# Kernel tuning notes

Hardware: AMD Instinct MI355X
Metric: run time of the kernel (lower is better)

Reference implementation:

```python
import jax, jax.numpy as jnp
import numpy as np

G, K = 60, 13  # SO(3) group size, neighbors per group element


def _gather(x, nei):
    # x: [N, C, G] -> [N, C, G, K] via fixed neighbor indices (len G*K)
    return x[:, :, nei].reshape(x.shape[0], x.shape[1], G, K)


def _comb(x, nei, W, b):
    # gather-then-(1,K)-Conv2d == contraction over (channel, neighbor)
    d = _gather(x, nei)                                   # [N,C,G,K]
    return jnp.einsum('ncgk,ock->nog', d, W) + b[None, :, None]


def setup_inputs() -> dict:
    key = jax.random.key(0)
    ks = jax.random.split(key, 8)
    N = 512
    feats = jax.random.normal(ks[0], (N, 32, G), jnp.float32)
    nei = jax.random.randint(ks[1], (G * K,), 0, G, jnp.int32)

    def w(k, o, c):
        return jax.random.normal(k, (o, c, K), jnp.float32) * (1.0 / np.sqrt(c * K))

    return {
        'feats': feats, 'nei': nei,
        'W_in': w(ks[2], 256, 32), 'b_in': jnp.zeros((256,), jnp.float32),
        'W_r1': w(ks[3], 512, 256), 'b_r1': jnp.zeros((512,), jnp.float32),
        'W_r2': w(ks[4], 256, 512), 'b_r2': jnp.zeros((256,), jnp.float32),
        'W_out': w(ks[5], 32, 256), 'b_out': jnp.zeros((32,), jnp.float32),
    }


def reference(feats, nei, W_in, b_in, W_r1, b_r1, W_r2, b_r2, W_out, b_out):
    # Conv_in: gather + (1,13) conv, 32 -> 256
    h = _comb(feats, nei, W_in, b_in)                      # [N,256,G]
    # Residual_Comb_Conv(256, 512, 256)
    r = jax.nn.relu(_comb(h, nei, W_r1, b_r1))             # [N,512,G]
    h = h + _comb(r, nei, W_r2, b_r2)                      # [N,256,G]
    # Conv_out: gather + (1,13) conv, 256 -> 32, then outer residual
    feats_eqv = _comb(h, nei, W_out, b_out) + feats        # [N,32,G]
    feats_inv = jnp.mean(feats_eqv, axis=-1)               # [N,32]
    feats_eqv = feats_eqv / jnp.maximum(
        jnp.linalg.norm(feats_eqv, axis=1, keepdims=True), 1e-4)
    feats_inv = feats_inv / jnp.maximum(
        jnp.linalg.norm(feats_inv, axis=1, keepdims=True), 1e-4)
    return feats_inv, feats_eqv
```

## Files before the change

### kernel.cpp

```cpp
#include <hip/hip_runtime.h>
#include <stdint.h>

#define GSZ 60
#define KNB 13
#define NPT 512

typedef __attribute__((ext_vector_type(4))) float f32x4;
typedef __attribute__((ext_vector_type(8))) short s16x8;

__device__ __forceinline__ ushort f2bf(float f) {
  union { float f; unsigned u; } v; v.f = f;
  unsigned r = v.u + 0x7fffu + ((v.u >> 16) & 1u);
  return (ushort)(r >> 16);
}
__device__ __forceinline__ float bf2f(ushort h) {
  union { unsigned u; float f; } v; v.u = ((unsigned)h) << 16;
  return v.f;
}

__device__ __forceinline__ void gload_lds16(const void* gsrc, void* ldst) {
  __builtin_amdgcn_global_load_lds(
      (const __attribute__((address_space(1))) uint32_t*)gsrc,
      (__attribute__((address_space(3))) uint32_t*)ldst, 16, 0, 0);
}

__global__ __launch_bounds__(256) void prep_feats_k(const float* __restrict__ feats,
                                                    ushort* __restrict__ X0) {
  int idx = blockIdx.x * 256 + threadIdx.x;
  if (idx >= 61 * NPT * 32) return;
  int c = idx & 31;
  int t = idx >> 5;
  int n = t % NPT;
  int g = t / NPT;
  X0[idx] = (g < GSZ) ? f2bf(feats[(n * 32 + c) * GSZ + g]) : (ushort)0;
}

__global__ __launch_bounds__(256) void prep_wb_k(const float* __restrict__ W,
                                                 ushort* __restrict__ Wb,
                                                 int O, int OPAD, int C, int KPAD) {
  int idx = blockIdx.x * 256 + threadIdx.x;
  if (idx >= OPAD * KPAD) return;
  int o = idx / KPAD;
  int kk = idx - o * KPAD;
  int k = kk / C;
  int c = kk - k * C;
  Wb[idx] = (o < O && k < KNB) ? f2bf(W[(o * C + c) * KNB + k]) : (ushort)0;
}

template <int CIN, int KTOT, int OPAD, int OREAL, int BN, int MODE, bool RELU>
__global__ __launch_bounds__(256) void comb_gemm(
    const ushort* __restrict__ Xin,
    const ushort* __restrict__ Wb,
    const float* __restrict__ bias,
    const int* __restrict__ nei,
    ushort* __restrict__ Xout,
    float* __restrict__ Eq,
    const float* __restrict__ feats)
{
  constexpr int BM = 128;
  constexpr int BK = 64;
  constexpr int NCH = KTOT / BK;
  constexpr int TO = OPAD / BN;
  constexpr int TN = NPT / BM;
  constexpr int WN = BN / 2;
  constexpr int N_REP = WN / 16;
  constexpr int M_REP = 4;
  constexpr int CSH = (CIN == 32) ? 5 : (CIN == 256) ? 8 : 9;
  static_assert(CIN == (1 << CSH), "CIN pow2");

  __shared__ ushort smA[BM * BK];
  __shared__ ushort smB[BN * BK];
  __shared__ int nei_sh[16];

  const int nwg = TO * TN * GSZ;
  const int cpx = nwg >> 3;
  const int bid = blockIdx.x;
  const int idx = (bid & 7) * cpx + (bid >> 3);
  const int g = idx / (TO * TN);
  const int rem = idx - g * (TO * TN);
  const int nt = rem / TO;
  const int ot = rem - nt * TO;
  const int n0 = nt * BM;
  const int o0 = ot * BN;

  const int t = threadIdx.x;
  if (t < 14) nei_sh[t] = (t < KNB) ? nei[g * KNB + t] : GSZ;
  __syncthreads();

  const int w = t >> 6;
  const int l = t & 63;
  const int lrow = l & 15;
  const int lkg = l >> 4;
  const int wr = w >> 1;
  const int wc = w & 1;
  const int srow_w = w * 8;
  const int sr = l >> 3;
  const int slot = l & 7;

  f32x4 acc[M_REP][N_REP] = {};

#pragma unroll 1
  for (int q = 0; q < NCH; ++q) {
    const int c0 = q * BK;
#pragma unroll
    for (int j = 0; j < BM / 32; ++j) {
      const int r = j * 32 + srow_w + sr;
      const int kk = c0 + ((slot ^ (r & 7)) << 3);
      const int nbr = kk >> CSH;
      const int cc = kk & (CIN - 1);
      const ushort* src = Xin + (((size_t)nei_sh[nbr] * NPT + n0 + r) << CSH) + cc;
      gload_lds16(src, &smA[(j * 32 + srow_w) * BK]);
    }
#pragma unroll
    for (int j = 0; j < BN / 32; ++j) {
      const int r = j * 32 + srow_w + sr;
      const int kk = c0 + ((slot ^ (r & 7)) << 3);
      const ushort* src = Wb + (size_t)(o0 + r) * KTOT + kk;
      gload_lds16(src, &smB[(j * 32 + srow_w) * BK]);
    }
    __syncthreads();
#pragma unroll
    for (int ks = 0; ks < 2; ++ks) {
      const int cb = ks * 4 + lkg;
      s16x8 bf[N_REP];
#pragma unroll
      for (int n = 0; n < N_REP; ++n) {
        const int r = wc * WN + n * 16 + lrow;
        bf[n] = *(const s16x8*)&smB[r * BK + ((cb ^ (r & 7)) << 3)];
      }
#pragma unroll
      for (int m = 0; m < M_REP; ++m) {
        const int r = wr * 64 + m * 16 + lrow;
        s16x8 af = *(const s16x8*)&smA[r * BK + ((cb ^ (r & 7)) << 3)];
#pragma unroll
        for (int n = 0; n < N_REP; ++n)
          acc[m][n] = __builtin_amdgcn_mfma_f32_16x16x32_bf16(af, bf[n], acc[m][n], 0, 0, 0);
      }
    }
    __syncthreads();
  }

#pragma unroll
  for (int m = 0; m < M_REP; ++m) {
#pragma unroll
    for (int n = 0; n < N_REP; ++n) {
      const int oc = o0 + wc * WN + n * 16 + lrow;
      float bv;
      if (MODE == 2)
        bv = (oc < OREAL) ? bias[oc] : 0.f;
      else
        bv = bias[oc];
#pragma unroll
      for (int r = 0; r < 4; ++r) {
        const int row = n0 + wr * 64 + m * 16 + lkg * 4 + r;
        float v = acc[m][n][r] + bv;
        if (MODE == 0) {
          if (RELU) v = v > 0.f ? v : 0.f;
          Xout[((size_t)g * NPT + row) * OPAD + oc] = f2bf(v);
        } else if (MODE == 1) {
          const size_t ix = ((size_t)g * NPT + row) * OPAD + oc;
          Xout[ix] = f2bf(bf2f(Xout[ix]) + v);
        } else {
          const float add = (oc < OREAL) ? feats[((size_t)row * 32 + oc) * GSZ + g] : 0.f;
          Eq[((size_t)g * NPT + row) * 64 + oc] = v + add;
        }
      }
    }
  }
}

__global__ __launch_bounds__(256) void finalize_k(const float* __restrict__ Eq,
                                                  float* __restrict__ out) {
  const int n = blockIdx.x;
  const int t = threadIdx.x;
  const int c = t & 31;
  const int gs = t >> 5;

  float invp = 0.f;
  for (int g = gs; g < GSZ; g += 8) {
    float x = Eq[((size_t)g * NPT + n) * 64 + c];
    invp += x;
    float ss = x * x;
#pragma unroll
    for (int m = 16; m >= 1; m >>= 1) ss += __shfl_xor(ss, m, 64);
    float nrm = sqrtf(ss);
    nrm = nrm > 1e-4f ? nrm : 1e-4f;
    out[16384 + ((size_t)n * 32 + c) * GSZ + g] = x / nrm;
  }

  __shared__ float tmp[8][32];
  tmp[gs][c] = invp;
  __syncthreads();
  if (t < 32) {
    float s = 0.f;
#pragma unroll
    for (int i = 0; i < 8; ++i) s += tmp[i][t];
    s *= (1.f / 60.f);
    float ss = s * s;
#pragma unroll
    for (int m = 16; m >= 1; m >>= 1) ss += __shfl_xor(ss, m, 64);
    float nrm = sqrtf(ss);
    nrm = nrm > 1e-4f ? nrm : 1e-4f;
    out[(size_t)n * 32 + t] = s / nrm;
  }
}

extern "C" void kernel_launch(void* const* d_in, const int* in_sizes, int n_in,
                              void* d_out, int out_size, void* d_ws, size_t ws_size,
                              hipStream_t stream) {
  const float* feats = (const float*)d_in[0];
  const int* nei = (const int*)d_in[1];
  const float* W_in = (const float*)d_in[2];
  const float* b_in = (const float*)d_in[3];
  const float* W_r1 = (const float*)d_in[4];
  const float* b_r1 = (const float*)d_in[5];
  const float* W_r2 = (const float*)d_in[6];
  const float* b_r2 = (const float*)d_in[7];
  const float* W_out = (const float*)d_in[8];
  const float* b_out = (const float*)d_in[9];
  float* out = (float*)d_out;

  char* ws = (char*)d_ws;
  size_t off = 0;
  auto alloc = [&](size_t bytes) {
    void* p = ws + off;
    off += (bytes + 255) & ~(size_t)255;
    return p;
  };
  ushort* X0 = (ushort*)alloc((size_t)61 * NPT * 32 * 2);
  ushort* H1 = (ushort*)alloc((size_t)GSZ * NPT * 256 * 2);
  ushort* R = (ushort*)alloc((size_t)GSZ * NPT * 512 * 2);
  float* Eq = (float*)alloc((size_t)GSZ * NPT * 64 * 4);
  ushort* Wb_in = (ushort*)alloc((size_t)256 * 448 * 2);
  ushort* Wb_r1 = (ushort*)alloc((size_t)512 * 3328 * 2);
  ushort* Wb_r2 = (ushort*)alloc((size_t)256 * 6656 * 2);
  ushort* Wb_out = (ushort*)alloc((size_t)64 * 3328 * 2);

  prep_feats_k<<<(61 * NPT * 32 + 255) / 256, 256, 0, stream>>>(feats, X0);
  prep_wb_k<<<(256 * 448 + 255) / 256, 256, 0, stream>>>(W_in, Wb_in, 256, 256, 32, 448);
  prep_wb_k<<<(512 * 3328 + 255) / 256, 256, 0, stream>>>(W_r1, Wb_r1, 512, 512, 256, 3328);
  prep_wb_k<<<(256 * 6656 + 255) / 256, 256, 0, stream>>>(W_r2, Wb_r2, 256, 256, 512, 6656);
  prep_wb_k<<<(64 * 3328 + 255) / 256, 256, 0, stream>>>(W_out, Wb_out, 32, 64, 256, 3328);

  dim3 blk(256);
  comb_gemm<32, 448, 256, 256, 128, 0, false><<<dim3(2 * 4 * GSZ), blk, 0, stream>>>(
      X0, Wb_in, b_in, nei, H1, nullptr, nullptr);
  comb_gemm<256, 3328, 512, 512, 128, 0, true><<<dim3(4 * 4 * GSZ), blk, 0, stream>>>(
      H1, Wb_r1, b_r1, nei, R, nullptr, nullptr);
  comb_gemm<512, 6656, 256, 256, 128, 1, false><<<dim3(2 * 4 * GSZ), blk, 0, stream>>>(
      R, Wb_r2, b_r2, nei, H1, nullptr, nullptr);
  comb_gemm<256, 3328, 64, 32, 64, 2, false><<<dim3(1 * 4 * GSZ), blk, 0, stream>>>(
      H1, Wb_out, b_out, nei, nullptr, Eq, feats);
  finalize_k<<<NPT, 256, 0, stream>>>(Eq, out);
}
```

Measured before the change: 355.8 us.

## Double-buffer LDS tiles to overlap global loads with MFMA compute

Adds a second LDS buffer for both A and B tiles and issues the next chunk's global-to-LDS loads before computing on the current one. The goal is to hide global load latency behind the MFMA work. It also precomputes per-lane address offsets outside the K loop, with a cheaper neighbor-base computation when CIN >= 64. In exchange, LDS use doubles, which may reduce occupancy, and the code relies on s_waitcnt plus a raw barrier for correctness.

```diff
diff --git a/kernel.cpp b/kernel.cpp
--- a/kernel.cpp
+++ b/kernel.cpp
@@ -68,8 +68,8 @@
   constexpr int CSH = (CIN == 32) ? 5 : (CIN == 256) ? 8 : 9;
   static_assert(CIN == (1 << CSH), "CIN pow2");
 
-  __shared__ ushort smA[BM * BK];
-  __shared__ ushort smB[BN * BK];
+  __shared__ ushort smA[2][BM * BK];
+  __shared__ ushort smB[2][BN * BK];
   __shared__ int nei_sh[16];
 
   const int nwg = TO * TN * GSZ;
@@ -97,28 +97,52 @@
   const int sr = l >> 3;
   const int slot = l & 7;
 
+  int laneA[BM / 32], laneB[BN / 32], swz[BM / 32];
+#pragma unroll
+  for (int j = 0; j < BM / 32; ++j) {
+    const int r = j * 32 + srow_w + sr;
+    swz[j] = (slot ^ (r & 7)) << 3;
+    laneA[j] = ((n0 + r) << CSH) + swz[j];
+  }
+#pragma unroll
+  for (int j = 0; j < BN / 32; ++j) {
+    const int r = j * 32 + srow_w + sr;
+    laneB[j] = (o0 + r) * KTOT + ((slot ^ (r & 7)) << 3);
+  }
+
+  auto stage = [&](int buf, int q) {
+    const int c0 = q * BK;
+    if constexpr (CIN >= 64) {
+      const int pbase = nei_sh[c0 >> CSH] * (NPT << CSH) + (c0 & (CIN - 1));
+#pragma unroll
+      for (int j = 0; j < BM / 32; ++j)
+        gload_lds16(Xin + pbase + laneA[j], &smA[buf][(j * 32 + srow_w) * BK]);
+    } else {
+#pragma unroll
+      for (int j = 0; j < BM / 32; ++j) {
+        const int r = j * 32 + srow_w + sr;
+        const int kk = c0 + swz[j];
+        const int nbr = kk >> CSH;
+        const int cc = kk & (CIN - 1);
+        gload_lds16(Xin + ((nei_sh[nbr] * NPT + n0 + r) << CSH) + cc,
+                    &smA[buf][(j * 32 + srow_w) * BK]);
+      }
+    }
+#pragma unroll
+    for (int j = 0; j < BN / 32; ++j)
+      gload_lds16(Wb + laneB[j] + c0, &smB[buf][(j * 32 + srow_w) * BK]);
+  };
+
   f32x4 acc[M_REP][N_REP] = {};
 
+  stage(0, 0);
+  asm volatile("s_waitcnt vmcnt(0)" ::: "memory");
+  __builtin_amdgcn_s_barrier();
+
+  int cur = 0;
 #pragma unroll 1
   for (int q = 0; q < NCH; ++q) {
-    const int c0 = q * BK;
-#pragma unroll
-    for (int j = 0; j < BM / 32; ++j) {
-      const int r = j * 32 + srow_w + sr;
-      const int kk = c0 + ((slot ^ (r & 7)) << 3);
-      const int nbr = kk >> CSH;
-      const int cc = kk & (CIN - 1);
-      const ushort* src = Xin + (((size_t)nei_sh[nbr] * NPT + n0 + r) << CSH) + cc;
-      gload_lds16(src, &smA[(j * 32 + srow_w) * BK]);
-    }
-#pragma unroll
-    for (int j = 0; j < BN / 32; ++j) {
-      const int r = j * 32 + srow_w + sr;
-      const int kk = c0 + ((slot ^ (r & 7)) << 3);
-      const ushort* src = Wb + (size_t)(o0 + r) * KTOT + kk;
-      gload_lds16(src, &smB[(j * 32 + srow_w) * BK]);
-    }
-    __syncthreads();
+    if (q + 1 < NCH) stage(cur ^ 1, q + 1);
 #pragma unroll
     for (int ks = 0; ks < 2; ++ks) {
       const int cb = ks * 4 + lkg;
@@ -126,18 +150,20 @@
 #pragma unroll
       for (int n = 0; n < N_REP; ++n) {
         const int r = wc * WN + n * 16 + lrow;
-        bf[n] = *(const s16x8*)&smB[r * BK + ((cb ^ (r & 7)) << 3)];
+        bf[n] = *(const s16x8*)&smB[cur][r * BK + ((cb ^ (r & 7)) << 3)];
       }
 #pragma unroll
       for (int m = 0; m < M_REP; ++m) {
         const int r = wr * 64 + m * 16 + lrow;
-        s16x8 af = *(const s16x8*)&smA[r * BK + ((cb ^ (r & 7)) << 3)];
+        s16x8 af = *(const s16x8*)&smA[cur][r * BK + ((cb ^ (r & 7)) << 3)];
 #pragma unroll
         for (int n = 0; n < N_REP; ++n)
           acc[m][n] = __builtin_amdgcn_mfma_f32_16x16x32_bf16(af, bf[n], acc[m][n], 0, 0, 0);
       }
     }
-    __syncthreads();
+    asm volatile("s_waitcnt vmcnt(0)" ::: "memory");
+    __builtin_amdgcn_s_barrier();
+    cur ^= 1;
   }
 
 #pragma unroll
```

Measured after the change: 325.3 us. 1.09x faster.
